# Kernel optimization log

Measured on AMD Instinct MI355X. Metric: run time of the kernel, lower is better.

The kernel has to match this reference:

```python
import jax, jax.numpy as jnp
import numpy as np

NUM_CLUSTERS = 16
GLOBAL_SCALE = 0.3
BETA0 = 1.0
NUM_ITERS = 10
LR = 0.5
SEED = 42  # module uses seed_int=42 when key is None


def _fps_init(x, mask_f, K, seed):
    """Farthest-point-sampling init of K means. x:(B,N,D), mask_f:(B,N) float."""
    B, N, D = x.shape
    start = seed % N
    first = x[:, start]                                   # (B,D)
    d2 = jnp.sum((x - first[:, None]) ** 2, axis=-1)      # (B,N)
    d2 = jnp.where(mask_f > 0, d2, -1.0)

    def step(d2c, _):
        idx = jnp.argmax(d2c, axis=1)                     # (B,)
        pt = jnp.take_along_axis(x, idx[:, None, None], axis=1)[:, 0]  # (B,D)
        nd = jnp.sum((x - pt[:, None]) ** 2, axis=-1)
        d2n = jnp.where(mask_f > 0, jnp.minimum(d2c, nd), -1.0)
        return d2n, pt

    _, pts = jax.lax.scan(step, d2, None, length=K - 1)   # (K-1,B,D)
    pts = jnp.moveaxis(pts, 0, 1)                         # (B,K-1,D)
    return jnp.concatenate([first[:, None], pts], axis=1)  # (B,K,D)


def _fit_vb_gmm(x, mask_f, K):
    """10-iteration damped VB-GMM EM. Returns means,covs,weights,valid,Nk."""
    B, N, D = x.shape
    current_N = jnp.sum(mask_f, axis=1)                   # (B,)
    N_eff = jnp.minimum(current_N, 40.0 * K)              # (B,)
    pw = mask_f * (N_eff / current_N)[:, None]            # (B,N) per-point weight
    sw = jnp.sum(pw, axis=1)                              # (B,) == N_eff

    m0 = jnp.sum(pw[..., None] * x, axis=1) / sw[:, None]                   # (B,D)
    var0 = jnp.sum(pw * jnp.sum((x - m0[:, None]) ** 2, -1), 1) / (sw * D)  # (B,)
    eye = jnp.eye(D, dtype=x.dtype)
    reg = (1e-4 * var0)[:, None, None, None] * eye                          # (B,1,D,D)

    means = _fps_init(x, mask_f, K, SEED)                                   # (B,K,D)
    covs = ((GLOBAL_SCALE ** 2) * var0)[:, None, None, None] * eye          # (B,1,D,D)
    covs = jnp.broadcast_to(covs, (B, K, D, D))
    weights = jnp.full((B, K), 1.0 / K, dtype=x.dtype)
    log2pi = jnp.log(2.0 * jnp.pi).astype(x.dtype)

    def em_step(carry, _):
        means, covs, weights = carry
        P = jnp.linalg.inv(covs)                          # (B,K,D,D)
        logdet = jnp.linalg.slogdet(covs)[1]              # (B,K)
        Pmu = jnp.einsum('bkde,bke->bkd', P, means)
        quad = (jnp.einsum('bnd,bkde,bne->bnk', x, P, x)
                - 2.0 * jnp.einsum('bnd,bkd->bnk', x, Pmu)
                + jnp.einsum('bkd,bkd->bk', means, Pmu)[:, None, :])
        logp = -0.5 * (quad + logdet[:, None, :] + D * log2pi)
        r = jax.nn.softmax(logp + jnp.log(weights + 1e-12)[:, None, :], axis=-1)
        wr = r * pw[:, :, None]                           # (B,N,K)
        Nk = jnp.sum(wr, axis=1) + 1e-8                   # (B,K)
        xbar = jnp.einsum('bnk,bnd->bkd', wr, x) / Nk[..., None]
        Exx = jnp.einsum('bnk,bnd,bne->bkde', wr, x, x) / Nk[..., None, None]
        S = Exx - xbar[..., :, None] * xbar[..., None, :]
        dm = xbar - m0[:, None]
        coef = (BETA0 / (BETA0 + Nk))[..., None, None]
        cov_new = S + coef * (dm[..., :, None] * dm[..., None, :]) + reg
        mu_new = (BETA0 * m0[:, None] + Nk[..., None] * xbar) / (BETA0 + Nk)[..., None]
        w_new = Nk / jnp.sum(Nk, axis=-1, keepdims=True)
        means = (1.0 - LR) * means + LR * mu_new
        covs = (1.0 - LR) * covs + LR * cov_new
        weights = (1.0 - LR) * weights + LR * w_new
        return (means, covs, weights), Nk

    (means, covs, weights), Nks = jax.lax.scan(em_step, (means, covs, weights), None, length=NUM_ITERS)
    Nk_last = Nks[-1]
    valid = (Nk_last > 1e-2 * N_eff[:, None] / K).astype(x.dtype)  # (B,K)
    return means, covs, weights, valid, Nk_last


def _forward(x, mask_f):
    B, N, D = x.shape
    K = NUM_CLUSTERS
    means, covs, weights, valid_mask, _ = _fit_vb_gmm(x, mask_f, K)
    e, v = jnp.linalg.eigh(covs)                          # (B,K,D),(B,K,D,D)
    sigma = jnp.sqrt(jnp.maximum(e, 0.0))
    scaled_vecs = v * sigma[..., None, :]                 # (B,K,D,D)
    axes_pos = means[..., :, None] + scaled_vecs
    axes_neg = means[..., :, None] - scaled_vecs
    coll = jnp.concatenate([means[..., :, None], axes_pos, axes_neg], axis=-1)  # (B,K,D,1+2D)
    coll = jnp.swapaxes(coll, -1, -2)                     # (B,K,1+2D,D)
    L = K * (1 + 2 * D)
    points_seq = coll.reshape(B, L, D)
    vm = jnp.repeat(valid_mask[:, :, None], 1 + 2 * D, axis=2).reshape(B, L)
    points_seq = points_seq * vm[:, :, None]
    return points_seq, vm


def setup_inputs() -> dict:
    key = jax.random.key(0)
    x = jax.random.normal(key, (64, 16384, 3), dtype=jnp.float32)
    mask = jnp.ones((64, 16384), dtype=bool)
    return {"x": x, "mask": mask}


def reference(x, mask):
    return _forward(x, mask.astype(x.dtype))
```

## Files before the change

### kernel.cpp

```cpp
#include <hip/hip_runtime.h>
#include <math.h>

namespace {

constexpr int kB    = 64;
constexpr int kN    = 16384;
constexpr int kK    = 16;
constexpr int kSUB  = 4;
constexpr int kETH  = 256;
constexpr int kEPT  = 16;

constexpr int WS_M0    = 0;
constexpr int WS_STATE = 256;
constexpr int WS_PART  = 256 + 64 * 160;

__device__ __forceinline__ float dist2nc(float ax, float ay, float az,
                                         float bx, float by, float bz) {
#pragma clang fp contract(off)
  float dx = ax - bx;
  float dy = ay - by;
  float dz = az - bz;
  float s2 = dx * dx + dy * dy;
  return s2 + dz * dz;
}

__device__ __forceinline__ float lapy2f(float x, float y) {
  float xa = fabsf(x), ya = fabsf(y);
  float w = fmaxf(xa, ya), z = fminf(xa, ya);
  if (z == 0.0f) return w;
  float t = z / w;
  return w * sqrtf(1.0f + t * t);
}

__device__ __forceinline__ void lartgf(float f, float g, float* cs, float* sn, float* r) {
  if (g == 0.0f) { *cs = 1.0f; *sn = 0.0f; *r = f; }
  else if (f == 0.0f) { *cs = 0.0f; *sn = copysignf(1.0f, g); *r = fabsf(g); }
  else {
    float d = sqrtf(f * f + g * g);
    float p = 1.0f / d;
    *cs = fabsf(f) * p;
    *sn = g * copysignf(p, f);
    *r  = copysignf(d, f);
  }
}

__device__ void laev2f(float a, float b, float c,
                       float* rt1, float* rt2, float* cs1, float* sn1) {
  float sm = a + c, df = a - c;
  float adf = fabsf(df), tb = b + b, ab = fabsf(tb);
  float acmx, acmn;
  if (fabsf(a) > fabsf(c)) { acmx = a; acmn = c; } else { acmx = c; acmn = a; }
  float rt;
  if (adf > ab)      { float t = ab / adf; rt = adf * sqrtf(1.0f + t * t); }
  else if (adf < ab) { float t = adf / ab; rt = ab * sqrtf(1.0f + t * t); }
  else               { rt = ab * sqrtf(2.0f); }
  int sgn1;
  if (sm < 0.0f) {
    *rt1 = 0.5f * (sm - rt); sgn1 = -1;
    *rt2 = (acmx / (*rt1)) * acmn - (b / (*rt1)) * b;
  } else if (sm > 0.0f) {
    *rt1 = 0.5f * (sm + rt); sgn1 = 1;
    *rt2 = (acmx / (*rt1)) * acmn - (b / (*rt1)) * b;
  } else {
    *rt1 = 0.5f * rt; *rt2 = -0.5f * rt; sgn1 = 1;
  }
  float cs; int sgn2;
  if (df >= 0.0f) { cs = df + rt; sgn2 = 1; } else { cs = df - rt; sgn2 = -1; }
  float acs = fabsf(cs), c1, s1;
  if (acs > ab) { float ct = -tb / cs; s1 = 1.0f / sqrtf(1.0f + ct * ct); c1 = ct * s1; }
  else {
    if (ab == 0.0f) { c1 = 1.0f; s1 = 0.0f; }
    else { float tn = -cs / tb; c1 = 1.0f / sqrtf(1.0f + tn * tn); s1 = tn * c1; }
  }
  if (sgn1 == sgn2) { float t = c1; c1 = -s1; s1 = t; }
  *cs1 = c1; *sn1 = s1;
}

__device__ void steqr3(float* dd, float* ee, float z[3][3]) {
  const float eps = 5.9604645e-8f;
  const float eps2 = eps * eps;
  const float safmin = 1.17549435e-38f;
  const int nmaxit = 90;
  int jtot = 0;
  int l1 = 1, l = 0, lsv, lend, lendsv, m, i;
  float p, g, r, c, s, f, bb, rt1, rt2;
  float cw[2], sw2[2];

L10:
  if (l1 > 3) goto L160;
  if (l1 > 1) ee[l1 - 2] = 0.0f;
  if (l1 <= 2) {
    for (m = l1; m <= 2; ++m) {
      float tst = fabsf(ee[m - 1]);
      if (tst == 0.0f) goto L30;
      if (tst <= (sqrtf(fabsf(dd[m - 1])) * sqrtf(fabsf(dd[m]))) * eps) {
        ee[m - 1] = 0.0f; goto L30;
      }
    }
  }
  m = 3;
L30:
  l = l1; lsv = l; lend = m; lendsv = lend; l1 = m + 1;
  if (lend == l) goto L10;
  {
    float anorm = 0.0f;
    for (i = l; i <= lend; ++i)      anorm = fmaxf(anorm, fabsf(dd[i - 1]));
    for (i = l; i <= lend - 1; ++i)  anorm = fmaxf(anorm, fabsf(ee[i - 1]));
    if (anorm == 0.0f) goto L10;
  }
  if (fabsf(dd[lend - 1]) < fabsf(dd[l - 1])) { lend = lsv; l = lendsv; }

  if (lend > l) {
L40:
    if (l != lend) {
      for (m = l; m <= lend - 1; ++m) {
        float tst = ee[m - 1] * ee[m - 1];
        if (tst <= (eps2 * fabsf(dd[m - 1])) * fabsf(dd[m]) + safmin) goto L60;
      }
    }
    m = lend;
L60:
    if (m < lend) ee[m - 1] = 0.0f;
    p = dd[l - 1];
    if (m == l) goto L80;
    if (m == l + 1) {
      laev2f(dd[l - 1], ee[l - 1], dd[l], &rt1, &rt2, &c, &s);
      for (int i2 = 0; i2 < 3; ++i2) {
        float temp = z[i2][l];
        z[i2][l]     = c * temp - s * z[i2][l - 1];
        z[i2][l - 1] = s * temp + c * z[i2][l - 1];
      }
      dd[l - 1] = rt1; dd[l] = rt2; ee[l - 1] = 0.0f;
      l += 2;
      if (l <= lend) goto L40;
      goto L140;
    }
    if (jtot == nmaxit) goto L140;
    jtot++;
    g = (dd[l] - p) / (2.0f * ee[l - 1]);
    r = lapy2f(g, 1.0f);
    g = dd[m - 1] - p + ee[l - 1] / (g + copysignf(r, g));
    s = 1.0f; c = 1.0f; p = 0.0f;
    for (i = m - 1; i >= l; --i) {
      f = s * ee[i - 1]; bb = c * ee[i - 1];
      lartgf(g, f, &c, &s, &r);
      if (i != m - 1) ee[i] = r;
      g = dd[i] - p;
      r = (dd[i - 1] - g) * s + 2.0f * c * bb;
      p = s * r;
      dd[i] = g + p;
      g = c * r - bb;
      cw[i - 1] = c; sw2[i - 1] = -s;
    }
    for (int jj = m - 1; jj >= l; --jj) {
      float ct = cw[jj - 1], st = sw2[jj - 1];
      for (int i2 = 0; i2 < 3; ++i2) {
        float temp = z[i2][jj];
        z[i2][jj]     = ct * temp - st * z[i2][jj - 1];
        z[i2][jj - 1] = st * temp + ct * z[i2][jj - 1];
      }
    }
    dd[l - 1] -= p;
    ee[l - 1] = g;
    goto L40;
L80:
    dd[l - 1] = p;
    l++;
    if (l <= lend) goto L40;
    goto L140;
  } else {
L90:
    if (l != lend) {
      for (m = l; m >= lend + 1; --m) {
        float tst = ee[m - 2] * ee[m - 2];
        if (tst <= (eps2 * fabsf(dd[m - 1])) * fabsf(dd[m - 2]) + safmin) goto L110;
      }
    }
    m = lend;
L110:
    if (m > lend) ee[m - 2] = 0.0f;
    p = dd[l - 1];
    if (m == l) goto L130;
    if (m == l - 1) {
      laev2f(dd[l - 2], ee[l - 2], dd[l - 1], &rt1, &rt2, &c, &s);
      for (int i2 = 0; i2 < 3; ++i2) {
        float temp = z[i2][l - 1];
        z[i2][l - 1] = c * temp - s * z[i2][l - 2];
        z[i2][l - 2] = s * temp + c * z[i2][l - 2];
      }
      dd[l - 2] = rt1; dd[l - 1] = rt2; ee[l - 2] = 0.0f;
      l -= 2;
      if (l >= lend) goto L90;
      goto L140;
    }
    if (jtot == nmaxit) goto L140;
    jtot++;
    g = (dd[l - 2] - p) / (2.0f * ee[l - 2]);
    r = lapy2f(g, 1.0f);
    g = dd[m - 1] - p + ee[l - 2] / (g + copysignf(r, g));
    s = 1.0f; c = 1.0f; p = 0.0f;
    for (i = m; i <= l - 1; ++i) {
      f = s * ee[i - 1]; bb = c * ee[i - 1];
      lartgf(g, f, &c, &s, &r);
      if (i != m) ee[i - 2] = r;
      g = dd[i - 1] - p;
      r = (dd[i] - g) * s + 2.0f * c * bb;
      p = s * r;
      dd[i - 1] = g + p;
      g = c * r - bb;
      cw[i - 1] = c; sw2[i - 1] = s;
    }
    for (int jj = m; jj <= l - 1; ++jj) {
      float ct = cw[jj - 1], st = sw2[jj - 1];
      for (int i2 = 0; i2 < 3; ++i2) {
        float temp = z[i2][jj];
        z[i2][jj]     = ct * temp - st * z[i2][jj - 1];
        z[i2][jj - 1] = st * temp + ct * z[i2][jj - 1];
      }
    }
    dd[l - 1] -= p;
    ee[l - 2] = g;
    goto L90;
L130:
    dd[l - 1] = p;
    l--;
    if (l >= lend) goto L90;
    goto L140;
  }
L140:
  if (jtot < nmaxit) goto L10;
  return;

L160:
  for (int ii = 2; ii <= 3; ++ii) {
    int i0 = ii - 1, k0 = i0;
    p = dd[i0 - 1];
    for (int j = ii; j <= 3; ++j) {
      if (dd[j - 1] < p) { k0 = j; p = dd[j - 1]; }
    }
    if (k0 != i0) {
      dd[k0 - 1] = dd[i0 - 1]; dd[i0 - 1] = p;
      for (i = 0; i < 3; ++i) {
        float t = z[i][i0 - 1]; z[i][i0 - 1] = z[i][k0 - 1]; z[i][k0 - 1] = t;
      }
    }
  }
}

__device__ void syevd3(const float* A, float* w, float z[3][3]) {
  float a00 = A[0], a01 = A[1], a02 = A[2], a11 = A[3], a12 = A[4], a22 = A[5];
  float d[3], e[2];
  float tau = 0.0f, v2 = 0.0f;

  float alpha = a01;
  float xnorm = fabsf(a02);
  if (xnorm == 0.0f) {
    tau = 0.0f; v2 = 0.0f;
    d[0] = a00; d[1] = a11; d[2] = a22; e[0] = a01; e[1] = a12;
  } else {
    float beta = -copysignf(lapy2f(alpha, xnorm), alpha);
    tau = (beta - alpha) / beta;
    v2  = a02 / (alpha - beta);
    float w1 = tau * (a11 + a12 * v2);
    float w2 = tau * (a12 + a22 * v2);
    float al = -0.5f * tau * (w1 + w2 * v2);
    w1 += al; w2 += al * v2;
    d[0] = a00;
    d[1] = a11 - w1 - w1;
    e[1] = a12 - w1 * v2 - w2;
    d[2] = a22 - v2 * w2 - w2 * v2;
    e[0] = beta;
  }

  for (int i = 0; i < 3; ++i)
    for (int j = 0; j < 3; ++j) z[i][j] = (i == j) ? 1.0f : 0.0f;

  steqr3(d, e, z);

  if (tau != 0.0f) {
    for (int j = 0; j < 3; ++j) {
      float s = z[1][j] + v2 * z[2][j];
      z[1][j] = z[1][j] - tau * s;
      z[2][j] = z[2][j] - tau * v2 * s;
    }
  }
  w[0] = d[0]; w[1] = d[1]; w[2] = d[2];
}

__global__ __launch_bounds__(1024, 1)
void setup_fps_kernel(const float* __restrict__ xg, float* __restrict__ ws) {
  const int b = blockIdx.x;
  const int tid = threadIdx.x;
  const int lane = tid & 63;
  const int wave = tid >> 6;
  const float* xb = xg + (size_t)b * (kN * 3);
  float* st = ws + WS_STATE + b * 160;

  __shared__ float s_redx[16], s_redy[16], s_redz[16];
  __shared__ float s_m0[3];
  __shared__ float s_var0;
  __shared__ float s_pt[3];
  __shared__ float s_val[16];
  __shared__ int   s_idx[16];

  float sx = 0.f, sy = 0.f, sz = 0.f;
#pragma unroll 4
  for (int c = 0; c < 16; ++c) {
    int n = c * 1024 + tid;
    sx += xb[3 * n + 0]; sy += xb[3 * n + 1]; sz += xb[3 * n + 2];
  }
#pragma unroll
  for (int o = 32; o >= 1; o >>= 1) {
    sx += __shfl_xor(sx, o); sy += __shfl_xor(sy, o); sz += __shfl_xor(sz, o);
  }
  if (lane == 0) { s_redx[wave] = sx; s_redy[wave] = sy; s_redz[wave] = sz; }
  __syncthreads();
  if (tid == 0) {
    float a = 0.f, b2 = 0.f, c2 = 0.f;
    for (int w = 0; w < 16; ++w) { a += s_redx[w]; b2 += s_redy[w]; c2 += s_redz[w]; }
    s_m0[0] = a / (float)kN; s_m0[1] = b2 / (float)kN; s_m0[2] = c2 / (float)kN;
  }
  __syncthreads();
  const float m00 = s_m0[0], m01 = s_m0[1], m02 = s_m0[2];

  float sv2 = 0.f;
#pragma unroll 4
  for (int c = 0; c < 16; ++c) {
    int n = c * 1024 + tid;
    float dx = xb[3 * n + 0] - m00, dy = xb[3 * n + 1] - m01, dz = xb[3 * n + 2] - m02;
    sv2 += dx * dx + dy * dy + dz * dz;
  }
#pragma unroll
  for (int o = 32; o >= 1; o >>= 1) sv2 += __shfl_xor(sv2, o);
  if (lane == 0) s_redx[wave] = sv2;
  __syncthreads();
  if (tid == 0) {
    float a = 0.f;
    for (int w = 0; w < 16; ++w) a += s_redx[w];
    s_var0 = a / (float)(3 * kN);
    ws[WS_M0 + b * 4 + 0] = m00;
    ws[WS_M0 + b * 4 + 1] = m01;
    ws[WS_M0 + b * 4 + 2] = m02;
    ws[WS_M0 + b * 4 + 3] = s_var0;
  }

  if (tid == 0) {
    s_pt[0] = xb[126]; s_pt[1] = xb[127]; s_pt[2] = xb[128];
    st[0] = xb[126]; st[1] = xb[127]; st[2] = xb[128];
  }
  __syncthreads();
  float d2[16];
  {
    float ax = s_pt[0], ay = s_pt[1], az = s_pt[2];
#pragma unroll 4
    for (int c = 0; c < 16; ++c) {
      int n = c * 1024 + tid;
      d2[c] = dist2nc(xb[3 * n + 0], xb[3 * n + 1], xb[3 * n + 2], ax, ay, az);
    }
  }

  for (int it = 1; it < kK; ++it) {
    float bv = -3.402823466e38f; int bi = 0x7fffffff;
#pragma unroll
    for (int c = 0; c < 16; ++c) {
      if (d2[c] > bv) { bv = d2[c]; bi = c * 1024 + tid; }
    }
#pragma unroll
    for (int o = 32; o >= 1; o >>= 1) {
      float ov = __shfl_xor(bv, o);
      int   oi = __shfl_xor(bi, o);
      if (ov > bv || (ov == bv && oi < bi)) { bv = ov; bi = oi; }
    }
    if (lane == 0) { s_val[wave] = bv; s_idx[wave] = bi; }
    __syncthreads();
    if (tid == 0) {
      float gv = s_val[0]; int gi = s_idx[0];
      for (int w = 1; w < 16; ++w) {
        float v = s_val[w]; int ii = s_idx[w];
        if (v > gv || (v == gv && ii < gi)) { gv = v; gi = ii; }
      }
      const float* pp = xb + (size_t)gi * 3;
      s_pt[0] = pp[0]; s_pt[1] = pp[1]; s_pt[2] = pp[2];
      st[it * 3 + 0] = pp[0]; st[it * 3 + 1] = pp[1]; st[it * 3 + 2] = pp[2];
    }
    __syncthreads();
    if (it < kK - 1) {
      float ax = s_pt[0], ay = s_pt[1], az = s_pt[2];
#pragma unroll 4
      for (int c = 0; c < 16; ++c) {
        int n = c * 1024 + tid;
        float nd = dist2nc(xb[3 * n + 0], xb[3 * n + 1], xb[3 * n + 2], ax, ay, az);
        d2[c] = fminf(d2[c], nd);
      }
    }
  }
}

__global__ __launch_bounds__(kETH, 1)
void em_step_kernel(const float* __restrict__ xg, float* __restrict__ ws, int iter) {
  const int batch = blockIdx.x >> 2;
  const int sub = blockIdx.x & 3;
  const int tid = threadIdx.x;
  const int lane = tid & 63;
  const int wave = tid >> 6;
  const float* xb = xg + (size_t)batch * (kN * 3);
  float* st = ws + WS_STATE + batch * 160;
  float* part = ws + WS_PART + (size_t)(batch * kSUB) * 160;

  __shared__ float s_cst[kK][10];
  __shared__ float s_Nk[kK];
  __shared__ float s_red[4 * 160];

  const float m00 = ws[WS_M0 + batch * 4 + 0];
  const float m01 = ws[WS_M0 + batch * 4 + 1];
  const float m02 = ws[WS_M0 + batch * 4 + 2];
  const float var0 = ws[WS_M0 + batch * 4 + 3];
  const float pwc = 0.0390625f;
  const float regv = 1e-4f * var0;

  float mu0, mu1, mu2, c00, c01, c02, c11, c12, c22, wk;
  if (tid < kK) {
    int k = tid;
    if (iter == 0) {
      mu0 = st[k * 3 + 0]; mu1 = st[k * 3 + 1]; mu2 = st[k * 3 + 2];
      float gs2 = 0.09f * var0;
      c00 = gs2; c01 = 0.f; c02 = 0.f; c11 = gs2; c12 = 0.f; c22 = gs2;
      wk = 0.0625f;
    } else {
      float mp0 = st[k * 3 + 0], mp1 = st[k * 3 + 1], mp2 = st[k * 3 + 2];
      float cp0 = st[48 + k * 6 + 0], cp1 = st[48 + k * 6 + 1], cp2 = st[48 + k * 6 + 2];
      float cp3 = st[48 + k * 6 + 3], cp4 = st[48 + k * 6 + 4], cp5 = st[48 + k * 6 + 5];
      float wp = st[144 + k];
      float mom[10];
#pragma unroll
      for (int j = 0; j < 10; ++j) {
        float a = part[0 * 160 + k * 10 + j];
        a += part[1 * 160 + k * 10 + j];
        a += part[2 * 160 + k * 10 + j];
        a += part[3 * 160 + k * 10 + j];
        mom[j] = a;
      }
      float Nk = pwc * mom[0] + 1e-8f;
      float xb0 = pwc * mom[1] / Nk;
      float xb1 = pwc * mom[2] / Nk;
      float xb2 = pwc * mom[3] / Nk;
      float E00 = pwc * mom[4] / Nk;
      float E01 = pwc * mom[5] / Nk;
      float E02 = pwc * mom[6] / Nk;
      float E11 = pwc * mom[7] / Nk;
      float E12 = pwc * mom[8] / Nk;
      float E22 = pwc * mom[9] / Nk;
      float S00 = E00 - xb0 * xb0, S01 = E01 - xb0 * xb1, S02 = E02 - xb0 * xb2;
      float S11 = E11 - xb1 * xb1, S12 = E12 - xb1 * xb2, S22 = E22 - xb2 * xb2;
      float dm0 = xb0 - m00, dm1 = xb1 - m01, dm2 = xb2 - m02;
      float coef = 1.0f / (1.0f + Nk);
      float cn00 = S00 + coef * (dm0 * dm0) + regv;
      float cn01 = S01 + coef * (dm0 * dm1);
      float cn02 = S02 + coef * (dm0 * dm2);
      float cn11 = S11 + coef * (dm1 * dm1) + regv;
      float cn12 = S12 + coef * (dm1 * dm2);
      float cn22 = S22 + coef * (dm2 * dm2) + regv;
      float bn = 1.0f + Nk;
      float mn0 = (m00 + Nk * xb0) / bn;
      float mn1 = (m01 + Nk * xb1) / bn;
      float mn2 = (m02 + Nk * xb2) / bn;
      mu0 = 0.5f * mp0 + 0.5f * mn0;
      mu1 = 0.5f * mp1 + 0.5f * mn1;
      mu2 = 0.5f * mp2 + 0.5f * mn2;
      c00 = 0.5f * cp0 + 0.5f * cn00;
      c01 = 0.5f * cp1 + 0.5f * cn01;
      c02 = 0.5f * cp2 + 0.5f * cn02;
      c11 = 0.5f * cp3 + 0.5f * cn11;
      c12 = 0.5f * cp4 + 0.5f * cn12;
      c22 = 0.5f * cp5 + 0.5f * cn22;
      s_Nk[k] = Nk;
      wk = wp;
    }
  }
  __syncthreads();
  if (tid < kK && iter > 0) {
    float sN = 0.f;
    for (int j = 0; j < kK; ++j) sN += s_Nk[j];
    wk = 0.5f * wk + 0.5f * (s_Nk[tid] / sN);
  }
  if (tid < kK) {
    int k = tid;
    float M0 = c11 * c22 - c12 * c12;
    float M1 = c01 * c22 - c12 * c02;
    float M2 = c01 * c12 - c11 * c02;
    float det = c00 * M0 - c01 * M1 + c02 * M2;
    float idet = 1.0f / det;
    float P00 = M0 * idet;
    float P01 = -M1 * idet;
    float P02 = M2 * idet;
    float P11 = (c00 * c22 - c02 * c02) * idet;
    float P12 = -(c00 * c12 - c02 * c01) * idet;
    float P22 = (c00 * c11 - c01 * c01) * idet;
    float logdet = logf(det);
    float Pm0 = P00 * mu0 + P01 * mu1 + P02 * mu2;
    float Pm1 = P01 * mu0 + P11 * mu1 + P12 * mu2;
    float Pm2 = P02 * mu0 + P12 * mu1 + P22 * mu2;
    float muPmu = mu0 * Pm0 + mu1 * Pm1 + mu2 * Pm2;
    float gk = logf(wk + 1e-12f) - 0.5f * (muPmu + logdet + 3.0f * 1.8378770351409912f);
    s_cst[k][0] = -0.5f * P00; s_cst[k][1] = -0.5f * P11; s_cst[k][2] = -0.5f * P22;
    s_cst[k][3] = -P01; s_cst[k][4] = -P02; s_cst[k][5] = -P12;
    s_cst[k][6] = Pm0;  s_cst[k][7] = Pm1;  s_cst[k][8] = Pm2;
    s_cst[k][9] = gk;
    if (sub == 0) {
      st[k * 3 + 0] = mu0; st[k * 3 + 1] = mu1; st[k * 3 + 2] = mu2;
      st[48 + k * 6 + 0] = c00; st[48 + k * 6 + 1] = c01; st[48 + k * 6 + 2] = c02;
      st[48 + k * 6 + 3] = c11; st[48 + k * 6 + 4] = c12; st[48 + k * 6 + 5] = c22;
      st[144 + k] = wk;
    }
  }
  __syncthreads();

  float cst[kK][10];
#pragma unroll
  for (int k = 0; k < kK; ++k)
#pragma unroll
    for (int j = 0; j < 10; ++j) cst[k][j] = s_cst[k][j];

  float acc[kK][10];
#pragma unroll
  for (int k = 0; k < kK; ++k)
#pragma unroll
    for (int j = 0; j < 10; ++j) acc[k][j] = 0.f;

  const int base = sub * (kN / kSUB) + tid;
  float cx = xb[3 * base + 0], cy = xb[3 * base + 1], cz = xb[3 * base + 2];
#pragma unroll 2
  for (int c = 0; c < kEPT; ++c) {
    float nx = 0.f, ny = 0.f, nz = 0.f;
    if (c + 1 < kEPT) {
      int n = base + (c + 1) * kETH;
      nx = xb[3 * n + 0]; ny = xb[3 * n + 1]; nz = xb[3 * n + 2];
    }
    float x0 = cx, x1 = cy, x2 = cz;
    float q00 = x0 * x0, q11 = x1 * x1, q22 = x2 * x2;
    float q01 = x0 * x1, q02 = x0 * x2, q12 = x1 * x2;
    float svv[kK];
#pragma unroll
    for (int k = 0; k < kK; ++k) {
      float t = cst[k][9];
      t = fmaf(cst[k][0], q00, t);
      t = fmaf(cst[k][1], q11, t);
      t = fmaf(cst[k][2], q22, t);
      t = fmaf(cst[k][3], q01, t);
      t = fmaf(cst[k][4], q02, t);
      t = fmaf(cst[k][5], q12, t);
      t = fmaf(cst[k][6], x0, t);
      t = fmaf(cst[k][7], x1, t);
      t = fmaf(cst[k][8], x2, t);
      svv[k] = t;
    }
    float mx = svv[0];
#pragma unroll
    for (int k = 1; k < kK; ++k) mx = fmaxf(mx, svv[k]);
    float ssum = 0.f;
#pragma unroll
    for (int k = 0; k < kK; ++k) { float e = __expf(svv[k] - mx); svv[k] = e; ssum += e; }
    float inv = 1.0f / ssum;
#pragma unroll
    for (int k = 0; k < kK; ++k) {
      float r = svv[k] * inv;
      acc[k][0] += r;
      acc[k][1] = fmaf(r, x0, acc[k][1]);
      acc[k][2] = fmaf(r, x1, acc[k][2]);
      acc[k][3] = fmaf(r, x2, acc[k][3]);
      acc[k][4] = fmaf(r, q00, acc[k][4]);
      acc[k][5] = fmaf(r, q01, acc[k][5]);
      acc[k][6] = fmaf(r, q02, acc[k][6]);
      acc[k][7] = fmaf(r, q11, acc[k][7]);
      acc[k][8] = fmaf(r, q12, acc[k][8]);
      acc[k][9] = fmaf(r, q22, acc[k][9]);
    }
    cx = nx; cy = ny; cz = nz;
  }

#pragma unroll
  for (int k = 0; k < kK; ++k)
#pragma unroll
    for (int j = 0; j < 10; ++j) {
      float v = acc[k][j];
#pragma unroll
      for (int o = 32; o >= 1; o >>= 1) v += __shfl_xor(v, o);
      acc[k][j] = v;
    }
  if (lane == 0) {
#pragma unroll
    for (int k = 0; k < kK; ++k)
#pragma unroll
      for (int j = 0; j < 10; ++j) s_red[wave * 160 + k * 10 + j] = acc[k][j];
  }
  __syncthreads();
  if (tid < 160) {
    float a = s_red[0 * 160 + tid];
    a += s_red[1 * 160 + tid];
    a += s_red[2 * 160 + tid];
    a += s_red[3 * 160 + tid];
    part[(size_t)sub * 160 + tid] = a;
  }
}

__global__ __launch_bounds__(1024, 1)
void finalize_kernel(float* __restrict__ ws, float* __restrict__ out) {
  const int b = blockIdx.x;
  const int tid = threadIdx.x;
  const int lane = tid & 63;
  const int wave = tid >> 6;
  float* st = ws + WS_STATE + b * 160;
  const float* part = ws + WS_PART + (size_t)(b * kSUB) * 160;

  __shared__ float s_mean[kK][3];
  __shared__ float s_cov[kK][6];
  __shared__ float s_Nk[kK];

  const float m00 = ws[WS_M0 + b * 4 + 0];
  const float m01 = ws[WS_M0 + b * 4 + 1];
  const float m02 = ws[WS_M0 + b * 4 + 2];
  const float var0 = ws[WS_M0 + b * 4 + 3];
  const float pwc = 0.0390625f;
  const float regv = 1e-4f * var0;

  if (tid < kK) {
    int k = tid;
    float mp0 = st[k * 3 + 0], mp1 = st[k * 3 + 1], mp2 = st[k * 3 + 2];
    float cp0 = st[48 + k * 6 + 0], cp1 = st[48 + k * 6 + 1], cp2 = st[48 + k * 6 + 2];
    float cp3 = st[48 + k * 6 + 3], cp4 = st[48 + k * 6 + 4], cp5 = st[48 + k * 6 + 5];
    float mom[10];
#pragma unroll
    for (int j = 0; j < 10; ++j) {
      float a = part[0 * 160 + k * 10 + j];
      a += part[1 * 160 + k * 10 + j];
      a += part[2 * 160 + k * 10 + j];
      a += part[3 * 160 + k * 10 + j];
      mom[j] = a;
    }
    float Nk = pwc * mom[0] + 1e-8f;
    float xb0 = pwc * mom[1] / Nk;
    float xb1 = pwc * mom[2] / Nk;
    float xb2 = pwc * mom[3] / Nk;
    float E00 = pwc * mom[4] / Nk;
    float E01 = pwc * mom[5] / Nk;
    float E02 = pwc * mom[6] / Nk;
    float E11 = pwc * mom[7] / Nk;
    float E12 = pwc * mom[8] / Nk;
    float E22 = pwc * mom[9] / Nk;
    float S00 = E00 - xb0 * xb0, S01 = E01 - xb0 * xb1, S02 = E02 - xb0 * xb2;
    float S11 = E11 - xb1 * xb1, S12 = E12 - xb1 * xb2, S22 = E22 - xb2 * xb2;
    float dm0 = xb0 - m00, dm1 = xb1 - m01, dm2 = xb2 - m02;
    float coef = 1.0f / (1.0f + Nk);
    float cn00 = S00 + coef * (dm0 * dm0) + regv;
    float cn01 = S01 + coef * (dm0 * dm1);
    float cn02 = S02 + coef * (dm0 * dm2);
    float cn11 = S11 + coef * (dm1 * dm1) + regv;
    float cn12 = S12 + coef * (dm1 * dm2);
    float cn22 = S22 + coef * (dm2 * dm2) + regv;
    float bn = 1.0f + Nk;
    float mn0 = (m00 + Nk * xb0) / bn;
    float mn1 = (m01 + Nk * xb1) / bn;
    float mn2 = (m02 + Nk * xb2) / bn;
    s_mean[k][0] = 0.5f * mp0 + 0.5f * mn0;
    s_mean[k][1] = 0.5f * mp1 + 0.5f * mn1;
    s_mean[k][2] = 0.5f * mp2 + 0.5f * mn2;
    s_cov[k][0] = 0.5f * cp0 + 0.5f * cn00;
    s_cov[k][1] = 0.5f * cp1 + 0.5f * cn01;
    s_cov[k][2] = 0.5f * cp2 + 0.5f * cn02;
    s_cov[k][3] = 0.5f * cp3 + 0.5f * cn11;
    s_cov[k][4] = 0.5f * cp4 + 0.5f * cn12;
    s_cov[k][5] = 0.5f * cp5 + 0.5f * cn22;
    s_Nk[k] = Nk;
  }
  __syncthreads();

  if (lane == 0 && wave < kK) {
    int k = wave;
    float A[6] = { s_cov[k][0], s_cov[k][1], s_cov[k][2],
                   s_cov[k][3], s_cov[k][4], s_cov[k][5] };
    float wv[3], Z[3][3];
    syevd3(A, wv, Z);
    const float thr = 0.01f * 640.0f / 16.0f;
    float valid = (s_Nk[k] > thr) ? 1.0f : 0.0f;
    float mu0 = s_mean[k][0], mu1 = s_mean[k][1], mu2 = s_mean[k][2];
    float sgs[3] = { sqrtf(fmaxf(wv[0], 0.0f)),
                     sqrtf(fmaxf(wv[1], 0.0f)),
                     sqrtf(fmaxf(wv[2], 0.0f)) };
    float* po = out + ((size_t)b * 112 + k * 7) * 3;
    po[0] = mu0 * valid; po[1] = mu1 * valid; po[2] = mu2 * valid;
#pragma unroll
    for (int i2 = 0; i2 < 3; ++i2) {
      float sgi = sgs[i2];
      po[(1 + i2) * 3 + 0] = (mu0 + Z[0][i2] * sgi) * valid;
      po[(1 + i2) * 3 + 1] = (mu1 + Z[1][i2] * sgi) * valid;
      po[(1 + i2) * 3 + 2] = (mu2 + Z[2][i2] * sgi) * valid;
      po[(4 + i2) * 3 + 0] = (mu0 - Z[0][i2] * sgi) * valid;
      po[(4 + i2) * 3 + 1] = (mu1 - Z[1][i2] * sgi) * valid;
      po[(4 + i2) * 3 + 2] = (mu2 - Z[2][i2] * sgi) * valid;
    }
    float* vo = out + (size_t)kB * 112 * 3 + (size_t)b * 112 + k * 7;
#pragma unroll
    for (int j = 0; j < 7; ++j) vo[j] = valid;
  }
}

}

extern "C" void kernel_launch(void* const* d_in, const int* in_sizes, int n_in,
                              void* d_out, int out_size, void* d_ws, size_t ws_size,
                              hipStream_t stream) {
  const float* x = (const float*)d_in[0];
  float* out = (float*)d_out;
  float* ws = (float*)d_ws;

  setup_fps_kernel<<<dim3(kB), dim3(1024), 0, stream>>>(x, ws);
  for (int it = 0; it < 10; ++it)
    em_step_kernel<<<dim3(kB * kSUB), dim3(kETH), 0, stream>>>(x, ws, it);
  finalize_kernel<<<dim3(kB), dim3(1024), 0, stream>>>(ws, out);
}
```

Baseline: 430.9 us.

## Split EM accumulation into cluster halves, double sub-blocks, cache FPS points in registers

The EM step kernel now splits each batch across 8 sub-blocks instead of 4, with 8 points per thread loaded up front. It does a first pass to get the softmax max and normaliser, then accumulates moments in two halves of 8 clusters each, recomputing the logits. This targets register pressure and spilling from holding 160 accumulators plus 160 constants, and doubles the grid for more parallelism, at the price of computing exp and logits twice. The partial-moment reduction moves to shared memory, and the FPS setup kernel keeps its 16 points per thread in registers instead of re-reading global memory each iteration.

```diff
diff --git a/kernel.cpp b/kernel.cpp
--- a/kernel.cpp
+++ b/kernel.cpp
@@ -6,9 +6,9 @@
 constexpr int kB    = 64;
 constexpr int kN    = 16384;
 constexpr int kK    = 16;
-constexpr int kSUB  = 4;
+constexpr int kSUB  = 8;
 constexpr int kETH  = 256;
-constexpr int kEPT  = 16;
+constexpr int kEPT  = 8;
 
 constexpr int WS_M0    = 0;
 constexpr int WS_STATE = 256;
@@ -22,6 +22,23 @@
   float dz = az - bz;
   float s2 = dx * dx + dy * dy;
   return s2 + dz * dz;
+}
+
+__device__ __forceinline__ float svv_eval(const float* c10,
+                                          float q00, float q11, float q22,
+                                          float q01, float q02, float q12,
+                                          float x0, float x1, float x2) {
+  float t = c10[9];
+  t = fmaf(c10[0], q00, t);
+  t = fmaf(c10[1], q11, t);
+  t = fmaf(c10[2], q22, t);
+  t = fmaf(c10[3], q01, t);
+  t = fmaf(c10[4], q02, t);
+  t = fmaf(c10[5], q12, t);
+  t = fmaf(c10[6], x0, t);
+  t = fmaf(c10[7], x1, t);
+  t = fmaf(c10[8], x2, t);
+  return t;
 }
 
 __device__ __forceinline__ float lapy2f(float x, float y) {
@@ -298,17 +315,23 @@
 
   __shared__ float s_redx[16], s_redy[16], s_redz[16];
   __shared__ float s_m0[3];
-  __shared__ float s_var0;
   __shared__ float s_pt[3];
   __shared__ float s_val[16];
   __shared__ int   s_idx[16];
-
-  float sx = 0.f, sy = 0.f, sz = 0.f;
-#pragma unroll 4
+  __shared__ int   s_gi;
+
+  float px[16], py[16], pz[16];
+#pragma unroll
   for (int c = 0; c < 16; ++c) {
     int n = c * 1024 + tid;
-    sx += xb[3 * n + 0]; sy += xb[3 * n + 1]; sz += xb[3 * n + 2];
-  }
+    px[c] = xb[3 * n + 0];
+    py[c] = xb[3 * n + 1];
+    pz[c] = xb[3 * n + 2];
+  }
+
+  float sx = 0.f, sy = 0.f, sz = 0.f;
+#pragma unroll
+  for (int c = 0; c < 16; ++c) { sx += px[c]; sy += py[c]; sz += pz[c]; }
 #pragma unroll
   for (int o = 32; o >= 1; o >>= 1) {
     sx += __shfl_xor(sx, o); sy += __shfl_xor(sy, o); sz += __shfl_xor(sz, o);
@@ -324,10 +347,9 @@
   const float m00 = s_m0[0], m01 = s_m0[1], m02 = s_m0[2];
 
   float sv2 = 0.f;
-#pragma unroll 4
+#pragma unroll
   for (int c = 0; c < 16; ++c) {
-    int n = c * 1024 + tid;
-    float dx = xb[3 * n + 0] - m00, dy = xb[3 * n + 1] - m01, dz = xb[3 * n + 2] - m02;
+    float dx = px[c] - m00, dy = py[c] - m01, dz = pz[c] - m02;
     sv2 += dx * dx + dy * dy + dz * dz;
   }
 #pragma unroll
@@ -337,26 +359,23 @@
   if (tid == 0) {
     float a = 0.f;
     for (int w = 0; w < 16; ++w) a += s_redx[w];
-    s_var0 = a / (float)(3 * kN);
     ws[WS_M0 + b * 4 + 0] = m00;
     ws[WS_M0 + b * 4 + 1] = m01;
     ws[WS_M0 + b * 4 + 2] = m02;
-    ws[WS_M0 + b * 4 + 3] = s_var0;
-  }
-
-  if (tid == 0) {
-    s_pt[0] = xb[126]; s_pt[1] = xb[127]; s_pt[2] = xb[128];
-    st[0] = xb[126]; st[1] = xb[127]; st[2] = xb[128];
+    ws[WS_M0 + b * 4 + 3] = a / (float)(3 * kN);
+  }
+
+  if (tid == 42) {
+    s_pt[0] = px[0]; s_pt[1] = py[0]; s_pt[2] = pz[0];
+    st[0] = px[0]; st[1] = py[0]; st[2] = pz[0];
   }
   __syncthreads();
   float d2[16];
   {
     float ax = s_pt[0], ay = s_pt[1], az = s_pt[2];
-#pragma unroll 4
-    for (int c = 0; c < 16; ++c) {
-      int n = c * 1024 + tid;
-      d2[c] = dist2nc(xb[3 * n + 0], xb[3 * n + 1], xb[3 * n + 2], ax, ay, az);
-    }
+#pragma unroll
+    for (int c = 0; c < 16; ++c)
+      d2[c] = dist2nc(px[c], py[c], pz[c], ax, ay, az);
   }
 
   for (int it = 1; it < kK; ++it) {
@@ -379,17 +398,25 @@
         float v = s_val[w]; int ii = s_idx[w];
         if (v > gv || (v == gv && ii < gi)) { gv = v; gi = ii; }
       }
-      const float* pp = xb + (size_t)gi * 3;
-      s_pt[0] = pp[0]; s_pt[1] = pp[1]; s_pt[2] = pp[2];
-      st[it * 3 + 0] = pp[0]; st[it * 3 + 1] = pp[1]; st[it * 3 + 2] = pp[2];
+      s_gi = gi;
+    }
+    __syncthreads();
+    {
+      int gi = s_gi;
+#pragma unroll
+      for (int c = 0; c < 16; ++c) {
+        if (c * 1024 + tid == gi) {
+          s_pt[0] = px[c]; s_pt[1] = py[c]; s_pt[2] = pz[c];
+          st[it * 3 + 0] = px[c]; st[it * 3 + 1] = py[c]; st[it * 3 + 2] = pz[c];
+        }
+      }
     }
     __syncthreads();
     if (it < kK - 1) {
       float ax = s_pt[0], ay = s_pt[1], az = s_pt[2];
-#pragma unroll 4
+#pragma unroll
       for (int c = 0; c < 16; ++c) {
-        int n = c * 1024 + tid;
-        float nd = dist2nc(xb[3 * n + 0], xb[3 * n + 1], xb[3 * n + 2], ax, ay, az);
+        float nd = dist2nc(px[c], py[c], pz[c], ax, ay, az);
         d2[c] = fminf(d2[c], nd);
       }
     }
@@ -398,8 +425,8 @@
 
 __global__ __launch_bounds__(kETH, 1)
 void em_step_kernel(const float* __restrict__ xg, float* __restrict__ ws, int iter) {
-  const int batch = blockIdx.x >> 2;
-  const int sub = blockIdx.x & 3;
+  const int batch = blockIdx.x >> 3;
+  const int sub = blockIdx.x & 7;
   const int tid = threadIdx.x;
   const int lane = tid & 63;
   const int wave = tid >> 6;
@@ -409,6 +436,7 @@
 
   __shared__ float s_cst[kK][10];
   __shared__ float s_Nk[kK];
+  __shared__ float s_mom[160];
   __shared__ float s_red[4 * 160];
 
   const float m00 = ws[WS_M0 + batch * 4 + 0];
@@ -417,6 +445,15 @@
   const float var0 = ws[WS_M0 + batch * 4 + 3];
   const float pwc = 0.0390625f;
   const float regv = 1e-4f * var0;
+
+  if (iter > 0) {
+    if (tid < 160) {
+      float a = 0.f;
+      for (int s = 0; s < kSUB; ++s) a += part[(size_t)s * 160 + tid];
+      s_mom[tid] = a;
+    }
+    __syncthreads();
+  }
 
   float mu0, mu1, mu2, c00, c01, c02, c11, c12, c22, wk;
   if (tid < kK) {
@@ -431,25 +468,16 @@
       float cp0 = st[48 + k * 6 + 0], cp1 = st[48 + k * 6 + 1], cp2 = st[48 + k * 6 + 2];
       float cp3 = st[48 + k * 6 + 3], cp4 = st[48 + k * 6 + 4], cp5 = st[48 + k * 6 + 5];
       float wp = st[144 + k];
-      float mom[10];
-#pragma unroll
-      for (int j = 0; j < 10; ++j) {
-        float a = part[0 * 160 + k * 10 + j];
-        a += part[1 * 160 + k * 10 + j];
-        a += part[2 * 160 + k * 10 + j];
-        a += part[3 * 160 + k * 10 + j];
-        mom[j] = a;
-      }
-      float Nk = pwc * mom[0] + 1e-8f;
-      float xb0 = pwc * mom[1] / Nk;
-      float xb1 = pwc * mom[2] / Nk;
-      float xb2 = pwc * mom[3] / Nk;
-      float E00 = pwc * mom[4] / Nk;
-      float E01 = pwc * mom[5] / Nk;
-      float E02 = pwc * mom[6] / Nk;
-      float E11 = pwc * mom[7] / Nk;
-      float E12 = pwc * mom[8] / Nk;
-      float E22 = pwc * mom[9] / Nk;
+      float Nk = pwc * s_mom[k * 10 + 0] + 1e-8f;
+      float xb0 = pwc * s_mom[k * 10 + 1] / Nk;
+      float xb1 = pwc * s_mom[k * 10 + 2] / Nk;
+      float xb2 = pwc * s_mom[k * 10 + 3] / Nk;
+      float E00 = pwc * s_mom[k * 10 + 4] / Nk;
+      float E01 = pwc * s_mom[k * 10 + 5] / Nk;
+      float E02 = pwc * s_mom[k * 10 + 6] / Nk;
+      float E11 = pwc * s_mom[k * 10 + 7] / Nk;
+      float E12 = pwc * s_mom[k * 10 + 8] / Nk;
+      float E22 = pwc * s_mom[k * 10 + 9] / Nk;
       float S00 = E00 - xb0 * xb0, S01 = E01 - xb0 * xb1, S02 = E02 - xb0 * xb2;
       float S11 = E11 - xb1 * xb1, S12 = E12 - xb1 * xb2, S22 = E22 - xb2 * xb2;
       float dm0 = xb0 - m00, dm1 = xb1 - m01, dm2 = xb2 - m02;
@@ -515,83 +543,95 @@
   }
   __syncthreads();
 
-  float cst[kK][10];
-#pragma unroll
-  for (int k = 0; k < kK; ++k)
-#pragma unroll
-    for (int j = 0; j < 10; ++j) cst[k][j] = s_cst[k][j];
-
-  float acc[kK][10];
-#pragma unroll
-  for (int k = 0; k < kK; ++k)
-#pragma unroll
-    for (int j = 0; j < 10; ++j) acc[k][j] = 0.f;
-
   const int base = sub * (kN / kSUB) + tid;
-  float cx = xb[3 * base + 0], cy = xb[3 * base + 1], cz = xb[3 * base + 2];
-#pragma unroll 2
-  for (int c = 0; c < kEPT; ++c) {
-    float nx = 0.f, ny = 0.f, nz = 0.f;
-    if (c + 1 < kEPT) {
-      int n = base + (c + 1) * kETH;
-      nx = xb[3 * n + 0]; ny = xb[3 * n + 1]; nz = xb[3 * n + 2];
-    }
-    float x0 = cx, x1 = cy, x2 = cz;
-    float q00 = x0 * x0, q11 = x1 * x1, q22 = x2 * x2;
-    float q01 = x0 * x1, q02 = x0 * x2, q12 = x1 * x2;
-    float svv[kK];
-#pragma unroll
-    for (int k = 0; k < kK; ++k) {
-      float t = cst[k][9];
-      t = fmaf(cst[k][0], q00, t);
-      t = fmaf(cst[k][1], q11, t);
-      t = fmaf(cst[k][2], q22, t);
-      t = fmaf(cst[k][3], q01, t);
-      t = fmaf(cst[k][4], q02, t);
-      t = fmaf(cst[k][5], q12, t);
-      t = fmaf(cst[k][6], x0, t);
-      t = fmaf(cst[k][7], x1, t);
-      t = fmaf(cst[k][8], x2, t);
-      svv[k] = t;
-    }
-    float mx = svv[0];
-#pragma unroll
-    for (int k = 1; k < kK; ++k) mx = fmaxf(mx, svv[k]);
-    float ssum = 0.f;
-#pragma unroll
-    for (int k = 0; k < kK; ++k) { float e = __expf(svv[k] - mx); svv[k] = e; ssum += e; }
-    float inv = 1.0f / ssum;
-#pragma unroll
-    for (int k = 0; k < kK; ++k) {
-      float r = svv[k] * inv;
-      acc[k][0] += r;
-      acc[k][1] = fmaf(r, x0, acc[k][1]);
-      acc[k][2] = fmaf(r, x1, acc[k][2]);
-      acc[k][3] = fmaf(r, x2, acc[k][3]);
-      acc[k][4] = fmaf(r, q00, acc[k][4]);
-      acc[k][5] = fmaf(r, q01, acc[k][5]);
-      acc[k][6] = fmaf(r, q02, acc[k][6]);
-      acc[k][7] = fmaf(r, q11, acc[k][7]);
-      acc[k][8] = fmaf(r, q12, acc[k][8]);
-      acc[k][9] = fmaf(r, q22, acc[k][9]);
-    }
-    cx = nx; cy = ny; cz = nz;
-  }
-
-#pragma unroll
-  for (int k = 0; k < kK; ++k)
-#pragma unroll
-    for (int j = 0; j < 10; ++j) {
-      float v = acc[k][j];
-#pragma unroll
-      for (int o = 32; o >= 1; o >>= 1) v += __shfl_xor(v, o);
-      acc[k][j] = v;
-    }
-  if (lane == 0) {
+  float px[kEPT], py[kEPT], pz[kEPT];
+#pragma unroll
+  for (int p = 0; p < kEPT; ++p) {
+    int n = base + p * kETH;
+    px[p] = xb[3 * n + 0]; py[p] = xb[3 * n + 1]; pz[p] = xb[3 * n + 2];
+  }
+
+  float mx[kEPT], minv[kEPT];
+  {
+    float cst[kK][10];
 #pragma unroll
     for (int k = 0; k < kK; ++k)
 #pragma unroll
-      for (int j = 0; j < 10; ++j) s_red[wave * 160 + k * 10 + j] = acc[k][j];
+      for (int j = 0; j < 10; ++j) cst[k][j] = s_cst[k][j];
+
+#pragma unroll
+    for (int p = 0; p < kEPT; ++p) {
+      float x0 = px[p], x1 = py[p], x2 = pz[p];
+      float q00 = x0 * x0, q11 = x1 * x1, q22 = x2 * x2;
+      float q01 = x0 * x1, q02 = x0 * x2, q12 = x1 * x2;
+      float svv[kK];
+#pragma unroll
+      for (int k = 0; k < kK; ++k)
+        svv[k] = svv_eval(cst[k], q00, q11, q22, q01, q02, q12, x0, x1, x2);
+      float m = svv[0];
+#pragma unroll
+      for (int k = 1; k < kK; ++k) m = fmaxf(m, svv[k]);
+      float ssum = 0.f;
+#pragma unroll
+      for (int k = 0; k < kK; ++k) { float e = __expf(svv[k] - m); ssum += e; }
+      mx[p] = m;
+      minv[p] = 1.0f / ssum;
+    }
+  }
+
+  for (int half = 0; half < 2; ++half) {
+    float cstc[8][10];
+#pragma unroll
+    for (int k = 0; k < 8; ++k)
+#pragma unroll
+      for (int j = 0; j < 10; ++j) cstc[k][j] = s_cst[half * 8 + k][j];
+
+    float acc[8][10];
+#pragma unroll
+    for (int k = 0; k < 8; ++k)
+#pragma unroll
+      for (int j = 0; j < 10; ++j) acc[k][j] = 0.f;
+
+#pragma unroll
+    for (int p = 0; p < kEPT; ++p) {
+      float x0 = px[p], x1 = py[p], x2 = pz[p];
+      float q00 = x0 * x0, q11 = x1 * x1, q22 = x2 * x2;
+      float q01 = x0 * x1, q02 = x0 * x2, q12 = x1 * x2;
+      float m = mx[p], iv = minv[p];
+#pragma unroll
+      for (int k = 0; k < 8; ++k) {
+        float t = svv_eval(cstc[k], q00, q11, q22, q01, q02, q12, x0, x1, x2);
+        float e = __expf(t - m);
+        float r = e * iv;
+        acc[k][0] += r;
+        acc[k][1] = fmaf(r, x0, acc[k][1]);
+        acc[k][2] = fmaf(r, x1, acc[k][2]);
+        acc[k][3] = fmaf(r, x2, acc[k][3]);
+        acc[k][4] = fmaf(r, q00, acc[k][4]);
+        acc[k][5] = fmaf(r, q01, acc[k][5]);
+        acc[k][6] = fmaf(r, q02, acc[k][6]);
+        acc[k][7] = fmaf(r, q11, acc[k][7]);
+        acc[k][8] = fmaf(r, q12, acc[k][8]);
+        acc[k][9] = fmaf(r, q22, acc[k][9]);
+      }
+    }
+
+#pragma unroll
+    for (int k = 0; k < 8; ++k)
+#pragma unroll
+      for (int j = 0; j < 10; ++j) {
+        float v = acc[k][j];
+#pragma unroll
+        for (int o = 32; o >= 1; o >>= 1) v += __shfl_xor(v, o);
+        acc[k][j] = v;
+      }
+    if (lane == 0) {
+#pragma unroll
+      for (int k = 0; k < 8; ++k)
+#pragma unroll
+        for (int j = 0; j < 10; ++j)
+          s_red[wave * 160 + (half * 8 + k) * 10 + j] = acc[k][j];
+    }
   }
   __syncthreads();
   if (tid < 160) {
@@ -612,6 +652,7 @@
   float* st = ws + WS_STATE + b * 160;
   const float* part = ws + WS_PART + (size_t)(b * kSUB) * 160;
 
+  __shared__ float s_mom[160];
   __shared__ float s_mean[kK][3];
   __shared__ float s_cov[kK][6];
   __shared__ float s_Nk[kK];
@@ -623,30 +664,28 @@
   const float pwc = 0.0390625f;
   const float regv = 1e-4f * var0;
 
+  if (tid < 160) {
+    float a = 0.f;
+    for (int s = 0; s < kSUB; ++s) a += part[(size_t)s * 160 + tid];
+    s_mom[tid] = a;
+  }
+  __syncthreads();
+
   if (tid < kK) {
     int k = tid;
     float mp0 = st[k * 3 + 0], mp1 = st[k * 3 + 1], mp2 = st[k * 3 + 2];
     float cp0 = st[48 + k * 6 + 0], cp1 = st[48 + k * 6 + 1], cp2 = st[48 + k * 6 + 2];
     float cp3 = st[48 + k * 6 + 3], cp4 = st[48 + k * 6 + 4], cp5 = st[48 + k * 6 + 5];
-    float mom[10];
-#pragma unroll
-    for (int j = 0; j < 10; ++j) {
-      float a = part[0 * 160 + k * 10 + j];
-      a += part[1 * 160 + k * 10 + j];
-      a += part[2 * 160 + k * 10 + j];
-      a += part[3 * 160 + k * 10 + j];
-      mom[j] = a;
-    }
-    float Nk = pwc * mom[0] + 1e-8f;
-    float xb0 = pwc * mom[1] / Nk;
-    float xb1 = pwc * mom[2] / Nk;
-    float xb2 = pwc * mom[3] / Nk;
-    float E00 = pwc * mom[4] / Nk;
-    float E01 = pwc * mom[5] / Nk;
-    float E02 = pwc * mom[6] / Nk;
-    float E11 = pwc * mom[7] / Nk;
-    float E12 = pwc * mom[8] / Nk;
-    float E22 = pwc * mom[9] / Nk;
+    float Nk = pwc * s_mom[k * 10 + 0] + 1e-8f;
+    float xb0 = pwc * s_mom[k * 10 + 1] / Nk;
+    float xb1 = pwc * s_mom[k * 10 + 2] / Nk;
+    float xb2 = pwc * s_mom[k * 10 + 3] / Nk;
+    float E00 = pwc * s_mom[k * 10 + 4] / Nk;
+    float E01 = pwc * s_mom[k * 10 + 5] / Nk;
+    float E02 = pwc * s_mom[k * 10 + 6] / Nk;
+    float E11 = pwc * s_mom[k * 10 + 7] / Nk;
+    float E12 = pwc * s_mom[k * 10 + 8] / Nk;
+    float E22 = pwc * s_mom[k * 10 + 9] / Nk;
     float S00 = E00 - xb0 * xb0, S01 = E01 - xb0 * xb1, S02 = E02 - xb0 * xb2;
     float S11 = E11 - xb1 * xb1, S12 = E12 - xb1 * xb2, S22 = E22 - xb2 * xb2;
     float dm0 = xb0 - m00, dm1 = xb1 - m01, dm2 = xb2 - m02;
```

Result: slower. 513.8 us (+19.2%).
